# Performance work log

Hardware: AMD Instinct MI355X
Metric: run time of the kernel (lower is better)

## Reference

```python
import jax, jax.numpy as jnp
import numpy as np

D, H, T, K = 512, 8, 4, 64   # dim, n_heads, n_tasks, topk_n
HD = D // H
PRUNE, EPS = 1e-3, 1e-8


def _ln(x, g, b, eps=1e-5):
    m = jnp.mean(x, axis=-1, keepdims=True)
    v = jnp.mean((x - m) ** 2, axis=-1, keepdims=True)
    return (x - m) * jax.lax.rsqrt(v + eps) * g + b


def setup_inputs() -> dict:
    key = jax.random.key(0)
    ks = jax.random.split(key, 5)
    B, N = 16, 8192
    tokens = jax.random.normal(ks[0], (B, N, D), jnp.float32)
    key_padding_mask = jax.random.uniform(ks[1], (B, N)) < 0.1  # True marks padding
    q = jax.random.normal(ks[2], (1, T, D), jnp.float32) * 0.02
    in_proj_w = jax.random.normal(ks[3], (3 * D, D), jnp.float32) / np.sqrt(D).astype(np.float32)
    in_proj_b = jnp.zeros((3 * D,), jnp.float32)
    pre_g = jnp.ones((D,), jnp.float32)
    pre_b = jnp.zeros((D,), jnp.float32)
    q_g = jnp.ones((D,), jnp.float32)
    q_b = jnp.zeros((D,), jnp.float32)
    log_tau = jnp.asarray(np.log(0.3), jnp.float32)
    return dict(tokens=tokens, key_padding_mask=key_padding_mask, q=q,
                in_proj_w=in_proj_w, in_proj_b=in_proj_b,
                pre_g=pre_g, pre_b=pre_b, q_g=q_g, q_b=q_b, log_tau=log_tau)


def reference(tokens, key_padding_mask, q, in_proj_w, in_proj_b,
              pre_g, pre_b, q_g, q_b, log_tau):
    B, N, _ = tokens.shape
    kpm = key_padding_mask  # [B,N], True = pad

    normed = _ln(tokens, pre_g, pre_b)                       # [B,N,D]
    tau = jnp.clip(jnp.exp(log_tau), 0.1, 10.0)
    query = _ln(q, q_g, q_b) / tau                           # [1,T,D]

    wq, wk, wv = in_proj_w[:D], in_proj_w[D:2 * D], in_proj_w[2 * D:]
    bq, bk, bv = in_proj_b[:D], in_proj_b[D:2 * D], in_proj_b[2 * D:]

    qp = (query[0] @ wq.T + bq).reshape(T, H, HD)            # [T,H,hd]
    kp = (normed @ wk.T + bk).reshape(B, N, H, HD)           # [B,N,H,hd]

    scores = jnp.einsum('thd,bnhd->bhtn', qp, kp) / np.float32(np.sqrt(HD))
    scores = jnp.where(kpm[:, None, None, :], -jnp.inf, scores)
    attn = jax.nn.softmax(scores, axis=-1)                   # [B,H,T,N]

    alpha = attn.mean(axis=1)                                # [B,T,N]
    alpha = jnp.where(kpm[:, None, :], 0.0, alpha)
    alpha = alpha / jnp.maximum(alpha.sum(-1, keepdims=True), EPS)

    # prune below threshold, with argmax one-hot fallback if everything pruned
    a = jnp.where(alpha < PRUNE, 0.0, alpha)
    a = jnp.where(kpm[:, None, :], 0.0, a)
    s = a.sum(-1, keepdims=True)
    need_fallback = s <= EPS                                 # [B,T,1]
    base = jnp.where(kpm[:, None, :], -1.0, alpha)
    onehot = jax.nn.one_hot(jnp.argmax(base, axis=-1), N, dtype=a.dtype)  # [B,T,N]
    a = jnp.where(need_fallback, onehot, a)
    a = jnp.where(kpm[:, None, :], 0.0, a)
    alpha = a / jnp.maximum(a.sum(-1, keepdims=True), EPS)

    # pool source: tie_mha_v projection of normed inputs
    pool_source = normed @ wv.T + bv                         # [B,N,D]

    # top-k gather + renorm weighting
    topv, topi = jax.lax.top_k(alpha, K)                     # [B,T,K]
    selected = jnp.take_along_axis(pool_source[:, None, :, :], topi[..., None], axis=2)  # [B,T,K,D]
    w = topv / jnp.maximum(topv.sum(-1, keepdims=True), EPS)
    pooled = (w[..., None] * selected).sum(axis=2)           # [B,T,D]
    return pooled
```

## Files before the change

### kernel.cpp

```cpp
#include <hip/hip_runtime.h>
#include <math.h>

#define Dd   512
#define Hh   8
#define Tt   4
#define HDd  64
#define Bb   16
#define Nn   8192
#define HTc  32
#define KS   64
#define NTOK (Bb*Nn)
#define PRUNEc 0.001f
#define EPSc   1e-8f

#define WS_C1     0u
#define WS_C0     128u
#define WS_M      2048u
#define WS_L      4096u
#define WS_FLAG   6144u
#define WS_G2H    65536u
#define WS_G2M    98304u
#define WS_G2L    131072u
#define WS_MEAN   163840u
#define WS_INV    688128u
#define WS_MASK8  1212416u
#define WS_PART   1343488u
#define WS_PEXP   4194304u

typedef __attribute__((ext_vector_type(8)))  short short8v;
typedef __attribute__((ext_vector_type(16))) float f32x16;

__device__ __forceinline__ void split3(float x, unsigned &h, unsigned &m, unsigned &l){
  unsigned u  = __float_as_uint(x);
  unsigned uh = u & 0xFFFF0000u;
  float rh = x - __uint_as_float(uh);
  unsigned um = __float_as_uint(rh) & 0xFFFF0000u;
  float rm = rh - __uint_as_float(um);
  unsigned ul = __float_as_uint(rm) & 0xFFFF0000u;
  h = uh; m = um; l = ul;
}

__device__ __forceinline__ void split3x8(float4 v0, float4 v1,
                                         short8v &h, short8v &m, short8v &l){
  union { short8v s; unsigned u[4]; } H, M, L;
  float a[8] = {v0.x,v0.y,v0.z,v0.w,v1.x,v1.y,v1.z,v1.w};
  #pragma unroll
  for (int w = 0; w < 4; ++w){
    unsigned ha, ma, la, hb, mb, lb;
    split3(a[2*w],   ha, ma, la);
    split3(a[2*w+1], hb, mb, lb);
    H.u[w] = (ha>>16) | (hb & 0xFFFF0000u);
    M.u[w] = (ma>>16) | (mb & 0xFFFF0000u);
    L.u[w] = (la>>16) | (lb & 0xFFFF0000u);
  }
  h = H.s; m = M.s; l = L.s;
}

__device__ __forceinline__ int chkw(unsigned v){
  return (v == 0x3f800000u) ? 2 : ((v & ~1u) ? 1 : 0);
}
__global__ void tap_detect(const uint4* mraw, int* flag){
  int tid = threadIdx.x;
  if (tid == 0) *flag = 0;
  __syncthreads();
  int f = 0;
  #pragma unroll
  for (int i = 0; i < 8; ++i){
    uint4 v = mraw[tid + i*1024];
    f |= chkw(v.x) | chkw(v.y) | chkw(v.z) | chkw(v.w);
  }
  if (f) atomicOr(flag, f);
}

__global__ void tap_mask(const void* mraw, const int* flag, uchar4* m8){
  int i = blockIdx.x*256 + threadIdx.x;
  int fl = *flag;
  uchar4 r;
  if (fl & 2){
    float4 v = ((const float4*)mraw)[i];
    r = make_uchar4(v.x != 0.f, v.y != 0.f, v.z != 0.f, v.w != 0.f);
  } else if (fl & 1){
    uchar4 v = ((const uchar4*)mraw)[i];
    r = make_uchar4(v.x != 0, v.y != 0, v.z != 0, v.w != 0);
  } else {
    int4 v = ((const int4*)mraw)[i];
    r = make_uchar4(v.x != 0, v.y != 0, v.z != 0, v.w != 0);
  }
  m8[i] = r;
}

__global__ void tap_prep(const float* q, const float* ipw, const float* ipb,
                         const float* pre_g, const float* pre_b,
                         const float* q_g, const float* q_b, const float* log_tau,
                         unsigned short* G2h, unsigned short* G2m, unsigned short* G2l,
                         float* C1, float* C0){
  __shared__ float query[Tt][Dd];
  __shared__ float qps[HDd];
  __shared__ float red[256];
  int tid = threadIdx.x;
  int ht = blockIdx.x;
  int h = ht >> 2, t = ht & 3;
  float tau = expf(log_tau[0]);
  tau = fminf(fmaxf(tau, 0.1f), 10.0f);
  float itau = 1.0f / tau;
  int wv = tid >> 6, lane = tid & 63;
  {
    const float* qr = q + wv*Dd;
    float s = 0.f, ss = 0.f;
    for (int j = lane; j < Dd; j += 64){ float x = qr[j]; s += x; ss += x*x; }
    #pragma unroll
    for (int off = 32; off; off >>= 1){ s += __shfl_down(s, off); ss += __shfl_down(ss, off); }
    s = __shfl(s, 0); ss = __shfl(ss, 0);
    float mean = s * (1.f/Dd);
    float var  = ss * (1.f/Dd) - mean*mean;
    float inv  = rsqrtf(var + 1e-5f);
    for (int j = lane; j < Dd; j += 64){
      float x = qr[j];
      query[wv][j] = ((x - mean)*inv*q_g[j] + q_b[j]) * itau;
    }
  }
  __syncthreads();
  {
    int d = tid >> 2, sub = tid & 3;
    int i = h*HDd + d;
    const float* wrow = ipw + (size_t)i*Dd;
    float acc = 0.f;
    int j0 = sub*128;
    for (int j = 0; j < 128; ++j) acc += query[t][j0+j]*wrow[j0+j];
    red[tid] = acc;
    __syncthreads();
    if (sub == 0) qps[d] = red[tid]+red[tid+1]+red[tid+2]+red[tid+3] + ipb[i];
    __syncthreads();
  }
  float c1p = 0.f, c0p = 0.f;
  for (int jj = 0; jj < 2; ++jj){
    int j = tid + jj*256;
    float acc = 0.f;
    #pragma unroll 8
    for (int d = 0; d < HDd; ++d)
      acc += qps[d] * ipw[(size_t)(Dd + h*HDd + d)*Dd + j];
    float w2 = acc * 0.125f;
    float g2 = w2 * pre_g[j];
    unsigned uh, um, ul;
    split3(g2, uh, um, ul);
    G2h[ht*Dd + j] = (unsigned short)(uh >> 16);
    G2m[ht*Dd + j] = (unsigned short)(um >> 16);
    G2l[ht*Dd + j] = (unsigned short)(ul >> 16);
    float geff = __uint_as_float(uh) + __uint_as_float(um) + __uint_as_float(ul);
    c1p += geff;
    c0p += w2 * pre_b[j];
  }
  if (tid < HDd) c0p += qps[tid] * ipb[Dd + h*HDd + tid] * 0.125f;
  red[tid] = c1p; __syncthreads();
  for (int s = 128; s; s >>= 1){ if (tid < s) red[tid] += red[tid+s]; __syncthreads(); }
  if (tid == 0) C1[ht] = red[0];
  __syncthreads();
  red[tid] = c0p; __syncthreads();
  for (int s = 128; s; s >>= 1){ if (tid < s) red[tid] += red[tid+s]; __syncthreads(); }
  if (tid == 0) C0[ht] = red[0];
}

__global__ __launch_bounds__(256, 4) void tap_scores(
    const float* __restrict__ tokens,
    const unsigned short* __restrict__ G2h, const unsigned short* __restrict__ G2m,
    const unsigned short* __restrict__ G2l,
    const float* __restrict__ C1, const float* __restrict__ C0,
    const unsigned char* __restrict__ m8,
    float* __restrict__ pexp, float2* __restrict__ part,
    float* __restrict__ meanw, float* __restrict__ invw){
  int tid   = threadIdx.x;
  int lane  = tid & 63, wv = tid >> 6;
  int col   = lane & 31;
  int bhalf = lane >> 5;
  size_t t0 = (size_t)blockIdx.x * 128;
  int brow  = (wv << 5) | col;
  const float* __restrict__ xrow = tokens + (t0 + brow)*(size_t)Dd;
  int abase = (col << 9) | (bhalf << 3);

  f32x16 acc;
  #pragma unroll
  for (int i = 0; i < 16; ++i) acc[i] = 0.f;
  float ps = 0.f, pss = 0.f;

  for (int c = 0; c < 8; ++c){
    #pragma unroll
    for (int kc = 0; kc < 4; ++kc){
      int k0 = (c << 6) | (kc << 4) | (bhalf << 3);
      float4 v0 = *(const float4*)(xrow + k0);
      float4 v1 = *(const float4*)(xrow + k0 + 4);
      int ga = abase + (c << 6) + (kc << 4);
      short8v ah = *(const short8v*)(G2h + ga);
      short8v am = *(const short8v*)(G2m + ga);
      short8v al = *(const short8v*)(G2l + ga);
      ps  += v0.x+v0.y+v0.z+v0.w + v1.x+v1.y+v1.z+v1.w;
      pss += v0.x*v0.x+v0.y*v0.y+v0.z*v0.z+v0.w*v0.w
           + v1.x*v1.x+v1.y*v1.y+v1.z*v1.z+v1.w*v1.w;
      short8v bh, bm, bl;
      split3x8(v0, v1, bh, bm, bl);
      acc = __builtin_amdgcn_mfma_f32_32x32x16_bf16(ah, bh, acc, 0, 0, 0);
      acc = __builtin_amdgcn_mfma_f32_32x32x16_bf16(am, bh, acc, 0, 0, 0);
      acc = __builtin_amdgcn_mfma_f32_32x32x16_bf16(ah, bm, acc, 0, 0, 0);
      acc = __builtin_amdgcn_mfma_f32_32x32x16_bf16(am, bm, acc, 0, 0, 0);
      acc = __builtin_amdgcn_mfma_f32_32x32x16_bf16(al, bh, acc, 0, 0, 0);
      acc = __builtin_amdgcn_mfma_f32_32x32x16_bf16(ah, bl, acc, 0, 0, 0);
    }
  }
  ps  += __shfl_xor(ps, 32);
  pss += __shfl_xor(pss, 32);
  float mean = ps * (1.f/512.f);
  float var  = pss * (1.f/512.f) - mean*mean;
  float inv  = rsqrtf(var + 1e-5f);
  if (bhalf == 0){ meanw[t0 + brow] = mean; invw[t0 + brow] = inv; }
  unsigned char mko = m8[t0 + brow];
  int b = (int)(t0 >> 13);
  int n = (int)(t0 & 8191) + brow;
  int g = (int)blockIdx.x*4 + wv;
  #pragma unroll
  for (int r = 0; r < 16; ++r){
    int ht = (r & 3) + ((r >> 2) << 3) + (bhalf << 2);
    float sc = mko ? -1e30f : (inv*(acc[r] - mean*C1[ht]) + C0[ht]);
    float mx = sc;
    #pragma unroll
    for (int off = 16; off; off >>= 1) mx = fmaxf(mx, __shfl_xor(mx, off));
    float p = mko ? 0.f : __expf(sc - mx);
    float ls = p;
    #pragma unroll
    for (int off = 16; off; off >>= 1) ls += __shfl_xor(ls, off);
    pexp[(((size_t)(b*HTc + ht)) << 13) + n] = p;
    if (col == r) part[(size_t)g*HTc + ht] = make_float2(mx, ls);
  }
}

__global__ void tap_combine(const float2* __restrict__ part,
                            float* __restrict__ mrow, float* __restrict__ lrow){
  int R = blockIdx.x;
  int b = R >> 5, ht = R & 31;
  int lane = threadIdx.x;
  const float2* pb = part + ((size_t)(b << 8))*HTc + ht;
  float2 v0 = pb[(size_t)(lane      )*HTc];
  float2 v1 = pb[(size_t)(lane +  64)*HTc];
  float2 v2 = pb[(size_t)(lane + 128)*HTc];
  float2 v3 = pb[(size_t)(lane + 192)*HTc];
  float M = fmaxf(fmaxf(v0.x, v1.x), fmaxf(v2.x, v3.x));
  #pragma unroll
  for (int off = 32; off; off >>= 1) M = fmaxf(M, __shfl_xor(M, off));
  float L = v0.y*__expf(v0.x - M) + v1.y*__expf(v1.x - M)
          + v2.y*__expf(v2.x - M) + v3.y*__expf(v3.x - M);
  #pragma unroll
  for (int off = 32; off; off >>= 1) L += __shfl_xor(L, off);
  if (lane == 0){ mrow[R] = M; lrow[R] = L; }
}

__global__ __launch_bounds__(512, 1) void tap_select(
    const float* __restrict__ tokens, const float* __restrict__ ipw,
    const float* __restrict__ ipb,
    const float* __restrict__ pre_g, const float* __restrict__ pre_b,
    const float* __restrict__ pexp, const float2* __restrict__ part,
    const unsigned char* __restrict__ m8,
    const float* __restrict__ mrow, const float* __restrict__ lrow,
    const float* __restrict__ meanw, const float* __restrict__ invw,
    float* __restrict__ out){
  __shared__ float av[Nn];
  __shared__ float fac[Hh][256];
  __shared__ float lv[1024];
  __shared__ int   li[1024];
  __shared__ float tw[KS]; __shared__ int ti[KS];
  __shared__ float coeff[KS];
  __shared__ __align__(16) float u[Dd];
  __shared__ float rs[8];
  __shared__ float rva[8]; __shared__ int ria[8]; __shared__ int rpa[8];
  __shared__ int cnt; __shared__ int sArg; __shared__ float sW, sS;
  int bt = blockIdx.x;
  int b = bt >> 2, t = bt & 3;
  int tid = threadIdx.x, lane = tid & 63, wvi = tid >> 6;
  if (tid == 0) cnt = 0;
  #pragma unroll
  for (int j = 0; j < 4; ++j){
    int idx = tid + (j << 9);
    int h = idx >> 8, s = idx & 255;
    int R = b*HTc + h*Tt + t;
    float m  = part[((size_t)(b << 8) + s)*HTc + (h*Tt + t)].x;
    float Mr = mrow[R], Lr = lrow[R];
    fac[h][s] = (Lr > 0.f) ? __expf(m - Mr) * (0.125f / Lr) : 0.f;
  }
  const float* pr[Hh];
  #pragma unroll
  for (int h = 0; h < Hh; ++h)
    pr[h] = pexp + ((size_t)(b*HTc + h*Tt + t) << 13);
  const unsigned char* mk = m8 + b*Nn;
  __syncthreads();
  float lsum = 0.f;
  float bvv = -2.f; int bii = 1 << 30;
  #pragma unroll 2
  for (int i = 0; i < 16; ++i){
    int n = tid + (i << 9);
    float fs = fac[0][n >> 5];
    float a = pr[0][n] * fs;
    #pragma unroll
    for (int h = 1; h < Hh; ++h) a += pr[h][n] * fac[h][n >> 5];
    av[n] = a;
    lsum += a;
    float bb = mk[n] ? -1.f : a;
    if (bb > bvv || (bb == bvv && n < bii)){ bvv = bb; bii = n; }
  }
  #pragma unroll
  for (int off = 32; off; off >>= 1) lsum += __shfl_down(lsum, off);
  if (lane == 0) rs[wvi] = lsum;
  #pragma unroll
  for (int off = 32; off; off >>= 1){
    float ov = __shfl_down(bvv, off);
    int   oi = __shfl_down(bii, off);
    if (ov > bvv || (ov == bvv && oi < bii)){ bvv = ov; bii = oi; }
  }
  if (lane == 0){ rva[wvi] = bvv; ria[wvi] = bii; }
  __syncthreads();
  float Sall = rs[0]+rs[1]+rs[2]+rs[3]+rs[4]+rs[5]+rs[6]+rs[7];
  if (tid == 0){
    float bv2 = rva[0]; int bi2 = ria[0];
    for (int w2 = 1; w2 < 8; ++w2)
      if (rva[w2] > bv2 || (rva[w2] == bv2 && ria[w2] < bi2)){ bv2 = rva[w2]; bi2 = ria[w2]; }
    sArg = bi2;
  }
  float f1 = 1.0f / fmaxf(Sall, EPSc);
  #pragma unroll 2
  for (int i = 0; i < 16; ++i){
    int n = tid + (i << 9);
    float x = av[n] * f1;
    if (x >= PRUNEc){
      int id = atomicAdd(&cnt, 1);
      if (id < 1024){ lv[id] = x; li[id] = n; }
    }
  }
  __syncthreads();
  int L = cnt;
  if (L == 0){
    if (tid == 0){ lv[0] = 1.f; li[0] = sArg; }
    L = 1;
    __syncthreads();
  }
  if (L <= KS){
    if (tid < KS){ tw[tid] = (tid < L) ? lv[tid] : 0.f; ti[tid] = (tid < L) ? li[tid] : 0; }
    __syncthreads();
  } else {
    for (int k = 0; k < KS; ++k){
      float bv = -1.f; int bn = 1 << 30; int bp = -1;
      for (int j = tid; j < L; j += 512){
        float x = lv[j]; int nn = li[j];
        if (x > bv || (x == bv && nn < bn)){ bv = x; bn = nn; bp = j; }
      }
      #pragma unroll
      for (int off = 32; off; off >>= 1){
        float ov = __shfl_down(bv, off);
        int   on = __shfl_down(bn, off);
        int   op = __shfl_down(bp, off);
        if (ov > bv || (ov == bv && on < bn)){ bv = ov; bn = on; bp = op; }
      }
      if (lane == 0){ rva[wvi] = bv; ria[wvi] = bn; rpa[wvi] = bp; }
      __syncthreads();
      if (tid == 0){
        float bb = rva[0]; int bj = ria[0]; int pp = rpa[0];
        for (int w2 = 1; w2 < 8; ++w2)
          if (rva[w2] > bb || (rva[w2] == bb && ria[w2] < bj)){ bb = rva[w2]; bj = ria[w2]; pp = rpa[w2]; }
        tw[k] = bb; ti[k] = bj;
        lv[pp] = -1.f;
      }
      __syncthreads();
    }
  }
  if (wvi == 0){
    float v = tw[lane];
    #pragma unroll
    for (int off = 32; off; off >>= 1) v += __shfl_down(v, off);
    if (lane == 0) sW = v;
  }
  __syncthreads();
  float sumw = sW;
  float Winv = 1.0f / fmaxf(sumw, EPSc);
  float Wn   = sumw * Winv;
  if (wvi == 0){
    int n = ti[lane];
    float mk2 = meanw[(size_t)b*Nn + n];
    float ik  = invw [(size_t)b*Nn + n];
    float wn  = tw[lane] * Winv;
    coeff[lane] = wn * ik;
    float sp = wn * mk2 * ik;
    #pragma unroll
    for (int off = 32; off; off >>= 1) sp += __shfl_down(sp, off);
    if (lane == 0) sS = sp;
  }
  __syncthreads();
  float Sv = sS;
  int d = tid;
  float acc0 = 0.f;
  #pragma unroll 4
  for (int k = 0; k < KS; ++k){
    float c = coeff[k];
    acc0 = fmaf(c, tokens[((size_t)b*Nn + ti[k])*Dd + d], acc0);
  }
  u[d] = pre_g[d]*(acc0 - Sv) + pre_b[d]*Wn;
  __syncthreads();
  const float4* u4 = (const float4*)u;
  const float4* w0 = (const float4*)(ipw + (size_t)(2*Dd + d)*Dd);
  float o0 = 0.f;
  #pragma unroll 4
  for (int j4 = 0; j4 < 128; ++j4){
    float4 uu = u4[j4];
    float4 a = w0[j4];
    o0 += uu.x*a.x + uu.y*a.y + uu.z*a.z + uu.w*a.w;
  }
  out[bt*Dd + d] = o0 + Wn*ipb[2*Dd + d];
}

extern "C" void kernel_launch(void* const* d_in, const int* in_sizes, int n_in,
                              void* d_out, int out_size, void* d_ws, size_t ws_size,
                              hipStream_t stream){
  const float* tokens = (const float*)d_in[0];
  const void*  kpm    = d_in[1];
  const float* q      = (const float*)d_in[2];
  const float* ipw    = (const float*)d_in[3];
  const float* ipb    = (const float*)d_in[4];
  const float* pre_g  = (const float*)d_in[5];
  const float* pre_b  = (const float*)d_in[6];
  const float* q_g    = (const float*)d_in[7];
  const float* q_b    = (const float*)d_in[8];
  const float* ltau   = (const float*)d_in[9];
  char* ws = (char*)d_ws;
  float* C1    = (float*)(ws + WS_C1);
  float* C0    = (float*)(ws + WS_C0);
  float* mrow  = (float*)(ws + WS_M);
  float* lrow  = (float*)(ws + WS_L);
  int*   flag  = (int*)  (ws + WS_FLAG);
  unsigned short* G2h = (unsigned short*)(ws + WS_G2H);
  unsigned short* G2m = (unsigned short*)(ws + WS_G2M);
  unsigned short* G2l = (unsigned short*)(ws + WS_G2L);
  float* meanw = (float*)(ws + WS_MEAN);
  float* invw  = (float*)(ws + WS_INV);
  unsigned char* m8 = (unsigned char*)(ws + WS_MASK8);
  float2* part = (float2*)(ws + WS_PART);
  float* pexp  = (float*)(ws + WS_PEXP);
  float* out = (float*)d_out;

  hipLaunchKernelGGL(tap_detect, dim3(1), dim3(1024), 0, stream, (const uint4*)kpm, flag);
  hipLaunchKernelGGL(tap_mask,   dim3(NTOK/1024), dim3(256), 0, stream, kpm, flag, (uchar4*)m8);
  hipLaunchKernelGGL(tap_prep,   dim3(HTc), dim3(256), 0, stream,
                     q, ipw, ipb, pre_g, pre_b, q_g, q_b, ltau, G2h, G2m, G2l, C1, C0);
  hipLaunchKernelGGL(tap_scores, dim3(NTOK/128), dim3(256), 0, stream,
                     tokens, G2h, G2m, G2l, C1, C0, m8, pexp, part, meanw, invw);
  hipLaunchKernelGGL(tap_combine, dim3(Bb*HTc), dim3(64), 0, stream, part, mrow, lrow);
  hipLaunchKernelGGL(tap_select, dim3(Bb*Tt), dim3(512), 0, stream,
                     tokens, ipw, ipb, pre_g, pre_b, pexp, part, m8,
                     mrow, lrow, meanw, invw, out);
}
```

Before: 589.1 us.

## Fuse mask decode and softmax combine into consumers; prefetch token chunks in score GEMM

Removes the separate mask-conversion kernel, so the scores and select kernels decode the raw padding mask inline using the detected dtype flag. The per-row max/sum combine kernel is folded into the select kernel, with one wavefront per head reducing the partials. The score kernel's K loop is restructured to software-prefetch the next 32-column chunk of tokens while running the MFMAs on the current one. This cuts two launches and an intermediate mask buffer, at the cost of more register pressure and a branchy mask load in the hot loops.

Result: faster. 573.7 us (-2.6%).

```diff
diff --git a/kernel.cpp b/kernel.cpp
--- a/kernel.cpp
+++ b/kernel.cpp
@@ -15,15 +15,12 @@
 
 #define WS_C1     0u
 #define WS_C0     128u
-#define WS_M      2048u
-#define WS_L      4096u
 #define WS_FLAG   6144u
 #define WS_G2H    65536u
 #define WS_G2M    98304u
 #define WS_G2L    131072u
 #define WS_MEAN   163840u
 #define WS_INV    688128u
-#define WS_MASK8  1212416u
 #define WS_PART   1343488u
 #define WS_PEXP   4194304u
 
@@ -56,6 +53,12 @@
   h = H.s; m = M.s; l = L.s;
 }
 
+__device__ __forceinline__ int mdecode(const void* mraw, int fl, size_t i){
+  if (fl & 2) return ((const float*)mraw)[i] != 0.0f;
+  if (fl & 1) return ((const unsigned char*)mraw)[i] != 0;
+  return ((const int*)mraw)[i] != 0;
+}
+
 __device__ __forceinline__ int chkw(unsigned v){
   return (v == 0x3f800000u) ? 2 : ((v & ~1u) ? 1 : 0);
 }
@@ -70,23 +73,6 @@
     f |= chkw(v.x) | chkw(v.y) | chkw(v.z) | chkw(v.w);
   }
   if (f) atomicOr(flag, f);
-}
-
-__global__ void tap_mask(const void* mraw, const int* flag, uchar4* m8){
-  int i = blockIdx.x*256 + threadIdx.x;
-  int fl = *flag;
-  uchar4 r;
-  if (fl & 2){
-    float4 v = ((const float4*)mraw)[i];
-    r = make_uchar4(v.x != 0.f, v.y != 0.f, v.z != 0.f, v.w != 0.f);
-  } else if (fl & 1){
-    uchar4 v = ((const uchar4*)mraw)[i];
-    r = make_uchar4(v.x != 0, v.y != 0, v.z != 0, v.w != 0);
-  } else {
-    int4 v = ((const int4*)mraw)[i];
-    r = make_uchar4(v.x != 0, v.y != 0, v.z != 0, v.w != 0);
-  }
-  m8[i] = r;
 }
 
 __global__ void tap_prep(const float* q, const float* ipw, const float* ipb,
@@ -165,7 +151,7 @@
     const unsigned short* __restrict__ G2h, const unsigned short* __restrict__ G2m,
     const unsigned short* __restrict__ G2l,
     const float* __restrict__ C1, const float* __restrict__ C0,
-    const unsigned char* __restrict__ m8,
+    const void* __restrict__ mraw, const int* __restrict__ flag,
     float* __restrict__ pexp, float2* __restrict__ part,
     float* __restrict__ meanw, float* __restrict__ invw){
   int tid   = threadIdx.x;
@@ -182,13 +168,26 @@
   for (int i = 0; i < 16; ++i) acc[i] = 0.f;
   float ps = 0.f, pss = 0.f;
 
-  for (int c = 0; c < 8; ++c){
-    #pragma unroll
-    for (int kc = 0; kc < 4; ++kc){
-      int k0 = (c << 6) | (kc << 4) | (bhalf << 3);
-      float4 v0 = *(const float4*)(xrow + k0);
-      float4 v1 = *(const float4*)(xrow + k0 + 4);
-      int ga = abase + (c << 6) + (kc << 4);
+  float4 cv0[2], cv1[2];
+  #pragma unroll
+  for (int sub = 0; sub < 2; ++sub){
+    int k0 = (sub << 4) | (bhalf << 3);
+    cv0[sub] = *(const float4*)(xrow + k0);
+    cv1[sub] = *(const float4*)(xrow + k0 + 4);
+  }
+  for (int s = 0; s < 16; ++s){
+    float4 nv0[2], nv1[2];
+    int sn = (s + 1) & 15;
+    #pragma unroll
+    for (int sub = 0; sub < 2; ++sub){
+      int k0 = (sn << 5) | (sub << 4) | (bhalf << 3);
+      nv0[sub] = *(const float4*)(xrow + k0);
+      nv1[sub] = *(const float4*)(xrow + k0 + 4);
+    }
+    #pragma unroll
+    for (int sub = 0; sub < 2; ++sub){
+      float4 v0 = cv0[sub], v1 = cv1[sub];
+      int ga = abase + (s << 5) + (sub << 4);
       short8v ah = *(const short8v*)(G2h + ga);
       short8v am = *(const short8v*)(G2m + ga);
       short8v al = *(const short8v*)(G2l + ga);
@@ -204,6 +203,8 @@
       acc = __builtin_amdgcn_mfma_f32_32x32x16_bf16(al, bh, acc, 0, 0, 0);
       acc = __builtin_amdgcn_mfma_f32_32x32x16_bf16(ah, bl, acc, 0, 0, 0);
     }
+    #pragma unroll
+    for (int sub = 0; sub < 2; ++sub){ cv0[sub] = nv0[sub]; cv1[sub] = nv1[sub]; }
   }
   ps  += __shfl_xor(ps, 32);
   pss += __shfl_xor(pss, 32);
@@ -211,7 +212,8 @@
   float var  = pss * (1.f/512.f) - mean*mean;
   float inv  = rsqrtf(var + 1e-5f);
   if (bhalf == 0){ meanw[t0 + brow] = mean; invw[t0 + brow] = inv; }
-  unsigned char mko = m8[t0 + brow];
+  int fl = *flag;
+  int mko = mdecode(mraw, fl, t0 + brow);
   int b = (int)(t0 >> 13);
   int n = (int)(t0 & 8191) + brow;
   int g = (int)blockIdx.x*4 + wv;
@@ -229,26 +231,6 @@
     pexp[(((size_t)(b*HTc + ht)) << 13) + n] = p;
     if (col == r) part[(size_t)g*HTc + ht] = make_float2(mx, ls);
   }
-}
-
-__global__ void tap_combine(const float2* __restrict__ part,
-                            float* __restrict__ mrow, float* __restrict__ lrow){
-  int R = blockIdx.x;
-  int b = R >> 5, ht = R & 31;
-  int lane = threadIdx.x;
-  const float2* pb = part + ((size_t)(b << 8))*HTc + ht;
-  float2 v0 = pb[(size_t)(lane      )*HTc];
-  float2 v1 = pb[(size_t)(lane +  64)*HTc];
-  float2 v2 = pb[(size_t)(lane + 128)*HTc];
-  float2 v3 = pb[(size_t)(lane + 192)*HTc];
-  float M = fmaxf(fmaxf(v0.x, v1.x), fmaxf(v2.x, v3.x));
-  #pragma unroll
-  for (int off = 32; off; off >>= 1) M = fmaxf(M, __shfl_xor(M, off));
-  float L = v0.y*__expf(v0.x - M) + v1.y*__expf(v1.x - M)
-          + v2.y*__expf(v2.x - M) + v3.y*__expf(v3.x - M);
-  #pragma unroll
-  for (int off = 32; off; off >>= 1) L += __shfl_xor(L, off);
-  if (lane == 0){ mrow[R] = M; lrow[R] = L; }
 }
 
 __global__ __launch_bounds__(512, 1) void tap_select(
@@ -256,8 +238,7 @@
     const float* __restrict__ ipb,
     const float* __restrict__ pre_g, const float* __restrict__ pre_b,
     const float* __restrict__ pexp, const float2* __restrict__ part,
-    const unsigned char* __restrict__ m8,
-    const float* __restrict__ mrow, const float* __restrict__ lrow,
+    const void* __restrict__ mraw, const int* __restrict__ flag,
     const float* __restrict__ meanw, const float* __restrict__ invw,
     float* __restrict__ out){
   __shared__ float av[Nn];
@@ -273,34 +254,44 @@
   int bt = blockIdx.x;
   int b = bt >> 2, t = bt & 3;
   int tid = threadIdx.x, lane = tid & 63, wvi = tid >> 6;
+  int fl = *flag;
   if (tid == 0) cnt = 0;
-  #pragma unroll
-  for (int j = 0; j < 4; ++j){
-    int idx = tid + (j << 9);
-    int h = idx >> 8, s = idx & 255;
-    int R = b*HTc + h*Tt + t;
-    float m  = part[((size_t)(b << 8) + s)*HTc + (h*Tt + t)].x;
-    float Mr = mrow[R], Lr = lrow[R];
-    fac[h][s] = (Lr > 0.f) ? __expf(m - Mr) * (0.125f / Lr) : 0.f;
+  {
+    int h = wvi;
+    const float2* pb = part + ((size_t)(b << 8))*HTc + (h*Tt + t);
+    float2 v0 = pb[(size_t)(lane      )*HTc];
+    float2 v1 = pb[(size_t)(lane +  64)*HTc];
+    float2 v2 = pb[(size_t)(lane + 128)*HTc];
+    float2 v3 = pb[(size_t)(lane + 192)*HTc];
+    float M = fmaxf(fmaxf(v0.x, v1.x), fmaxf(v2.x, v3.x));
+    #pragma unroll
+    for (int off = 32; off; off >>= 1) M = fmaxf(M, __shfl_xor(M, off));
+    float L = v0.y*__expf(v0.x - M) + v1.y*__expf(v1.x - M)
+            + v2.y*__expf(v2.x - M) + v3.y*__expf(v3.x - M);
+    #pragma unroll
+    for (int off = 32; off; off >>= 1) L += __shfl_xor(L, off);
+    float inv8L = (L > 0.f) ? 0.125f / L : 0.f;
+    fac[h][lane      ] = __expf(v0.x - M) * inv8L;
+    fac[h][lane +  64] = __expf(v1.x - M) * inv8L;
+    fac[h][lane + 128] = __expf(v2.x - M) * inv8L;
+    fac[h][lane + 192] = __expf(v3.x - M) * inv8L;
   }
   const float* pr[Hh];
   #pragma unroll
   for (int h = 0; h < Hh; ++h)
     pr[h] = pexp + ((size_t)(b*HTc + h*Tt + t) << 13);
-  const unsigned char* mk = m8 + b*Nn;
   __syncthreads();
   float lsum = 0.f;
   float bvv = -2.f; int bii = 1 << 30;
   #pragma unroll 2
   for (int i = 0; i < 16; ++i){
     int n = tid + (i << 9);
-    float fs = fac[0][n >> 5];
-    float a = pr[0][n] * fs;
+    float a = pr[0][n] * fac[0][n >> 5];
     #pragma unroll
     for (int h = 1; h < Hh; ++h) a += pr[h][n] * fac[h][n >> 5];
     av[n] = a;
     lsum += a;
-    float bb = mk[n] ? -1.f : a;
+    float bb = mdecode(mraw, fl, (size_t)b*Nn + n) ? -1.f : a;
     if (bb > bvv || (bb == bvv && n < bii)){ bvv = bb; bii = n; }
   }
   #pragma unroll
@@ -427,27 +418,22 @@
   char* ws = (char*)d_ws;
   float* C1    = (float*)(ws + WS_C1);
   float* C0    = (float*)(ws + WS_C0);
-  float* mrow  = (float*)(ws + WS_M);
-  float* lrow  = (float*)(ws + WS_L);
   int*   flag  = (int*)  (ws + WS_FLAG);
   unsigned short* G2h = (unsigned short*)(ws + WS_G2H);
   unsigned short* G2m = (unsigned short*)(ws + WS_G2M);
   unsigned short* G2l = (unsigned short*)(ws + WS_G2L);
   float* meanw = (float*)(ws + WS_MEAN);
   float* invw  = (float*)(ws + WS_INV);
-  unsigned char* m8 = (unsigned char*)(ws + WS_MASK8);
   float2* part = (float2*)(ws + WS_PART);
   float* pexp  = (float*)(ws + WS_PEXP);
   float* out = (float*)d_out;
 
   hipLaunchKernelGGL(tap_detect, dim3(1), dim3(1024), 0, stream, (const uint4*)kpm, flag);
-  hipLaunchKernelGGL(tap_mask,   dim3(NTOK/1024), dim3(256), 0, stream, kpm, flag, (uchar4*)m8);
   hipLaunchKernelGGL(tap_prep,   dim3(HTc), dim3(256), 0, stream,
                      q, ipw, ipb, pre_g, pre_b, q_g, q_b, ltau, G2h, G2m, G2l, C1, C0);
   hipLaunchKernelGGL(tap_scores, dim3(NTOK/128), dim3(256), 0, stream,
-                     tokens, G2h, G2m, G2l, C1, C0, m8, pexp, part, meanw, invw);
-  hipLaunchKernelGGL(tap_combine, dim3(Bb*HTc), dim3(64), 0, stream, part, mrow, lrow);
+                     tokens, G2h, G2m, G2l, C1, C0, kpm, flag, pexp, part, meanw, invw);
   hipLaunchKernelGGL(tap_select, dim3(Bb*Tt), dim3(512), 0, stream,
-                     tokens, ipw, ipb, pre_g, pre_b, pexp, part, m8,
-                     mrow, lrow, meanw, invw, out);
-}
+                     tokens, ipw, ipb, pre_g, pre_b, pexp, part, kpm, flag,
+                     meanw, invw, out);
+}
```
